# Optimization experiments

Hardware: AMD Instinct MI355X
Metric: run time of the kernel (lower is better)

The kernel has to match this reference:

```python
import jax, jax.numpy as jnp
import numpy as np


def setup_inputs() -> dict:
    key = jax.random.key(0)
    k1, k2 = jax.random.split(key)
    B, T, F, S, C = 16, 1024, 8, 128, 256
    e_src = jax.random.normal(k1, (B, T, F, C), dtype=jnp.float32)
    d_src = jax.random.randint(k2, (B, S), 0, 16, dtype=jnp.int64)
    return {"e_src": e_src, "d_src": d_src}


def reference(e_src, d_src):
    # Ragged per-phone mean pooling (the nested python loop in FastSpeech2Pros.forward):
    # e_src: [B, T_mel, F, C]; d_src: [B, S] frame durations per phone.
    # For b in range(B//2): chunk e_src[b] along T by durations, mean over (time, freq),
    # zeros for empty chunks -> agg [B//2, S, C].
    B, T, F, C = e_src.shape
    Bh = B // 2
    S = d_src.shape[1]
    e = e_src[:Bh]                      # [Bh, T, F, C]
    d = d_src[:Bh].astype(jnp.int32)    # [Bh, S]

    # frame t belongs to phone i iff cumsum(d)[i-1] <= t < cumsum(d)[i]
    cum = jnp.cumsum(d, axis=1)                                   # [Bh, S]
    t = jnp.arange(T, dtype=jnp.int32)
    seg = jax.vmap(lambda c: jnp.searchsorted(c, t, side='right'))(cum)  # [Bh, T]
    seg = jnp.minimum(seg, S)           # frames beyond total duration -> overflow bucket S

    frame_sum = e.sum(axis=2)           # [Bh, T, C] (sum over freq dim)
    sums = jax.vmap(
        lambda fs, s: jax.ops.segment_sum(fs, s, num_segments=S + 1)
    )(frame_sum, seg)[:, :S]            # [Bh, S, C]

    counts = (d * F).astype(e.dtype)    # elements per ragged chunk = dur * F
    agg = jnp.where(counts[..., None] > 0,
                    sums / jnp.maximum(counts, 1.0)[..., None],
                    jnp.zeros((), e.dtype))
    return agg
```

## Files before the change

### kernel.cpp

```cpp
#include <hip/hip_runtime.h>

#define TT 1024
#define SS 128
#define FF 8
#define CC 256
#define BH 8

__global__ __launch_bounds__(256) void fused_kernel(const float* __restrict__ e,
                                                    const int* __restrict__ dsrc,
                                                    float* __restrict__ out) {
    int s = blockIdx.x;
    int b = blockIdx.y;
    int tid = threadIdx.x;
    int c4 = tid & 63;
    int q  = tid >> 6;

    __shared__ int cumbuf[SS];
    if (tid < SS) cumbuf[tid] = dsrc[b * SS + tid];
    __syncthreads();
    #pragma unroll
    for (int off = 1; off < SS; off <<= 1) {
        int v = 0;
        if (tid < SS && tid >= off) v = cumbuf[tid - off];
        __syncthreads();
        if (tid < SS) cumbuf[tid] += v;
        __syncthreads();
    }

    int end   = cumbuf[s];
    int start = (s == 0) ? 0 : cumbuf[s - 1];
    int dc    = dsrc[b * SS + s];
    if (start > TT) start = TT;
    if (end   > TT) end   = TT;
    int K = (end - start) * FF;

    const float4* e4 = (const float4*)(e + (size_t)(b * TT + start) * (FF * CC));

    float ax = 0.f, ay = 0.f, az = 0.f, aw = 0.f;
    int k = q;
    for (; k + 12 < K; k += 16) {
        float4 v0 = e4[(size_t)(k     ) * 64 + c4];
        float4 v1 = e4[(size_t)(k +  4) * 64 + c4];
        float4 v2 = e4[(size_t)(k +  8) * 64 + c4];
        float4 v3 = e4[(size_t)(k + 12) * 64 + c4];
        ax += v0.x + v1.x + v2.x + v3.x;
        ay += v0.y + v1.y + v2.y + v3.y;
        az += v0.z + v1.z + v2.z + v3.z;
        aw += v0.w + v1.w + v2.w + v3.w;
    }
    for (; k < K; k += 4) {
        float4 v = e4[(size_t)k * 64 + c4];
        ax += v.x; ay += v.y; az += v.z; aw += v.w;
    }

    __shared__ float4 red[256];
    red[tid] = make_float4(ax, ay, az, aw);
    __syncthreads();

    if (q == 0) {
        float4 r0 = red[tid];
        float4 r1 = red[tid + 64];
        float4 r2 = red[tid + 128];
        float4 r3 = red[tid + 192];
        float inv = (dc > 0) ? (1.0f / (float)(dc * FF)) : 0.0f;
        float4 r;
        r.x = (r0.x + r1.x + r2.x + r3.x) * inv;
        r.y = (r0.y + r1.y + r2.y + r3.y) * inv;
        r.z = (r0.z + r1.z + r2.z + r3.z) * inv;
        r.w = (r0.w + r1.w + r2.w + r3.w) * inv;
        ((float4*)out)[(size_t)(b * SS + s) * 64 + c4] = r;
    }
}

extern "C" void kernel_launch(void* const* d_in, const int* in_sizes, int n_in,
                              void* d_out, int out_size, void* d_ws, size_t ws_size,
                              hipStream_t stream) {
    const float* e   = (const float*)d_in[0];
    const int*   d   = (const int*)d_in[1];
    float*       out = (float*)d_out;

    fused_kernel<<<dim3(SS, BH), 256, 0, stream>>>(e, d, out);
}
```

Measured before the change: 175.8 us.

## Split into prep and time-tiled segment-sum kernels with atomic accumulation

```diff
diff --git a/kernel.cpp b/kernel.cpp
--- a/kernel.cpp
+++ b/kernel.cpp
@@ -5,71 +5,93 @@
 #define FF 8
 #define CC 256
 #define BH 8
+#define TB 8
 
-__global__ __launch_bounds__(256) void fused_kernel(const float* __restrict__ e,
-                                                    const int* __restrict__ dsrc,
-                                                    float* __restrict__ out) {
-    int s = blockIdx.x;
-    int b = blockIdx.y;
+
+__global__ __launch_bounds__(256) void prep_kernel(const int* __restrict__ dsrc,
+                                                   int* __restrict__ segt,
+                                                   float* __restrict__ invt,
+                                                   float4* __restrict__ outz) {
     int tid = threadIdx.x;
-    int c4 = tid & 63;
-    int q  = tid >> 6;
+    int gid = blockIdx.x * 256 + tid;
+    outz[gid] = make_float4(0.f, 0.f, 0.f, 0.f);
+    if (blockIdx.x != 0) return;
 
-    __shared__ int cumbuf[SS];
-    if (tid < SS) cumbuf[tid] = dsrc[b * SS + tid];
+    __shared__ int dl[BH * SS];
+    __shared__ int cum[BH][SS];
+    for (int i = tid; i < BH * SS; i += 256) dl[i] = dsrc[i];
     __syncthreads();
-    #pragma unroll
-    for (int off = 1; off < SS; off <<= 1) {
-        int v = 0;
-        if (tid < SS && tid >= off) v = cumbuf[tid - off];
-        __syncthreads();
-        if (tid < SS) cumbuf[tid] += v;
-        __syncthreads();
+    if (tid < BH) {
+        int a = 0;
+        for (int s = 0; s < SS; ++s) { a += dl[tid * SS + s]; cum[tid][s] = a; }
+    }
+    __syncthreads();
+    for (int i = tid; i < BH * SS; i += 256) {
+        int d = dl[i];
+        invt[i] = (d > 0) ? 1.0f / (float)(d * FF) : 0.0f;
+    }
+    for (int i = tid; i < BH * TT; i += 256) {
+        int b = i >> 10, t = i & (TT - 1);
+        int lo = 0, hi = SS;
+        while (lo < hi) { int mid = (lo + hi) >> 1; if (cum[b][mid] <= t) lo = mid + 1; else hi = mid; }
+        segt[i] = lo;
+    }
+}
+
+#define FLUSH(SEG)                                                                        \
+    {                                                                                     \
+        red[tid] = acc; __syncthreads();                                                  \
+        if (tid < 64) {                                                                   \
+            float4 a0 = red[tid], a1 = red[tid + 64], a2 = red[tid + 128], a3 = red[tid + 192]; \
+            float inv = invt[b * SS + (SEG)];                                             \
+            float* o = out + ((size_t)(b * SS + (SEG)) * CC) + tid * 4;                   \
+            unsafeAtomicAdd(o + 0, (a0.x + a1.x + a2.x + a3.x) * inv);                    \
+            unsafeAtomicAdd(o + 1, (a0.y + a1.y + a2.y + a3.y) * inv);                    \
+            unsafeAtomicAdd(o + 2, (a0.z + a1.z + a2.z + a3.z) * inv);                    \
+            unsafeAtomicAdd(o + 3, (a0.w + a1.w + a2.w + a3.w) * inv);                    \
+        }                                                                                 \
+        __syncthreads();                                                                  \
     }
 
-    int end   = cumbuf[s];
-    int start = (s == 0) ? 0 : cumbuf[s - 1];
-    int dc    = dsrc[b * SS + s];
-    if (start > TT) start = TT;
-    if (end   > TT) end   = TT;
-    int K = (end - start) * FF;
+__global__ __launch_bounds__(256) void sum_kernel(const float* __restrict__ e,
+                                                  const int* __restrict__ segt,
+                                                  const float* __restrict__ invt,
+                                                  float* __restrict__ out) {
+    int t0  = blockIdx.x * TB;
+    int b   = blockIdx.y;
+    int tid = threadIdx.x;
 
-    const float4* e4 = (const float4*)(e + (size_t)(b * TT + start) * (FF * CC));
+    const int* st = segt + b * TT + t0;
+    int seg[TB];
+    #pragma unroll
+    for (int m = 0; m < TB; ++m) seg[m] = st[m];
+    if (seg[0] >= SS) return;
 
-    float ax = 0.f, ay = 0.f, az = 0.f, aw = 0.f;
-    int k = q;
-    for (; k + 12 < K; k += 16) {
-        float4 v0 = e4[(size_t)(k     ) * 64 + c4];
-        float4 v1 = e4[(size_t)(k +  4) * 64 + c4];
-        float4 v2 = e4[(size_t)(k +  8) * 64 + c4];
-        float4 v3 = e4[(size_t)(k + 12) * 64 + c4];
-        ax += v0.x + v1.x + v2.x + v3.x;
-        ay += v0.y + v1.y + v2.y + v3.y;
-        az += v0.z + v1.z + v2.z + v3.z;
-        aw += v0.w + v1.w + v2.w + v3.w;
-    }
-    for (; k < K; k += 4) {
-        float4 v = e4[(size_t)k * 64 + c4];
-        ax += v.x; ay += v.y; az += v.z; aw += v.w;
-    }
+    const float4* e4 = (const float4*)e + (size_t)(b * TT + t0) * (FF * CC / 4);
+    float4 v[16];
+    #pragma unroll
+    for (int j = 0; j < 16; ++j) v[j] = e4[j * 256 + tid];
 
     __shared__ float4 red[256];
-    red[tid] = make_float4(ax, ay, az, aw);
-    __syncthreads();
-
-    if (q == 0) {
-        float4 r0 = red[tid];
-        float4 r1 = red[tid + 64];
-        float4 r2 = red[tid + 128];
-        float4 r3 = red[tid + 192];
-        float inv = (dc > 0) ? (1.0f / (float)(dc * FF)) : 0.0f;
-        float4 r;
-        r.x = (r0.x + r1.x + r2.x + r3.x) * inv;
-        r.y = (r0.y + r1.y + r2.y + r3.y) * inv;
-        r.z = (r0.z + r1.z + r2.z + r3.z) * inv;
-        r.w = (r0.w + r1.w + r2.w + r3.w) * inv;
-        ((float4*)out)[(size_t)(b * SS + s) * 64 + c4] = r;
+    float4 acc = make_float4(0.f, 0.f, 0.f, 0.f);
+    int cur = seg[0];
+    #pragma unroll
+    for (int m = 0; m < TB; ++m) {
+        int s = seg[m];
+        if (s != cur) {
+            FLUSH(cur);
+            acc = make_float4(0.f, 0.f, 0.f, 0.f);
+            cur = s;
+        }
+        if (s < SS) {
+            float4 va = v[2 * m], vb = v[2 * m + 1];
+            acc.x += va.x + vb.x;
+            acc.y += va.y + vb.y;
+            acc.z += va.z + vb.z;
+            acc.w += va.w + vb.w;
+        }
     }
+    if (cur < SS) FLUSH(cur);
 }
 
 extern "C" void kernel_launch(void* const* d_in, const int* in_sizes, int n_in,
@@ -79,5 +101,9 @@
     const int*   d   = (const int*)d_in[1];
     float*       out = (float*)d_out;
 
-    fused_kernel<<<dim3(SS, BH), 256, 0, stream>>>(e, d, out);
+    int*   segt = (int*)d_ws;
+    float* invt = (float*)((char*)d_ws + (size_t)BH * TT * sizeof(int));
+
+    prep_kernel<<<dim3(256), 256, 0, stream>>>(d, segt, invt, (float4*)out);
+    sum_kernel<<<dim3(TT / TB, BH), 256, 0, stream>>>(e, segt, invt, out);
 }
```

Measured after the change: 193.5 us. 10.0% more time.

## Partition work by time frames with atomic accumulation into zeroed output

Applied to the files above, without the earlier changes.

```diff
diff --git a/kernel.cpp b/kernel.cpp
--- a/kernel.cpp
+++ b/kernel.cpp
@@ -5,70 +5,76 @@
 #define FF 8
 #define CC 256
 #define BH 8
+#define TB 8
+
+__global__ __launch_bounds__(256) void zero_kernel(float4* __restrict__ out) {
+    out[blockIdx.x * 256 + threadIdx.x] = make_float4(0.f, 0.f, 0.f, 0.f);
+}
+
+__device__ __forceinline__ void flush_seg(float* __restrict__ out, int b, int s,
+                                          int d0, int d1, int lane, float4 acc) {
+    int dsel = (s & 1) ? d1 : d0;
+    int ds   = __shfl(dsel, s >> 1, 64);
+    float inv = 1.0f / (float)(ds * FF);
+    float* o = out + ((size_t)(b * SS + s) * CC) + lane * 4;
+    unsafeAtomicAdd(o + 0, acc.x * inv);
+    unsafeAtomicAdd(o + 1, acc.y * inv);
+    unsafeAtomicAdd(o + 2, acc.z * inv);
+    unsafeAtomicAdd(o + 3, acc.w * inv);
+}
 
 __global__ __launch_bounds__(256) void fused_kernel(const float* __restrict__ e,
                                                     const int* __restrict__ dsrc,
                                                     float* __restrict__ out) {
-    int s = blockIdx.x;
-    int b = blockIdx.y;
-    int tid = threadIdx.x;
-    int c4 = tid & 63;
-    int q  = tid >> 6;
+    int x    = blockIdx.x;
+    int b    = blockIdx.y;
+    int tid  = threadIdx.x;
+    int lane = tid & 63;
+    int q    = tid >> 6;
 
-    __shared__ int cumbuf[SS];
-    if (tid < SS) cumbuf[tid] = dsrc[b * SS + tid];
-    __syncthreads();
+    int2 dd = ((const int2*)(dsrc + b * SS))[lane];
+    int incl = dd.x + dd.y;
     #pragma unroll
-    for (int off = 1; off < SS; off <<= 1) {
-        int v = 0;
-        if (tid < SS && tid >= off) v = cumbuf[tid - off];
-        __syncthreads();
-        if (tid < SS) cumbuf[tid] += v;
-        __syncthreads();
+    for (int off = 1; off < 64; off <<= 1) {
+        int n = __shfl_up(incl, off, 64);
+        if (lane >= off) incl += n;
+    }
+    int cumO = incl;
+    int cumE = incl - dd.y;
+
+    int tA = x * TB + 2 * q;
+    int tB = tA + 1;
+    int segA = __popcll(__ballot(cumE <= tA)) + __popcll(__ballot(cumO <= tA));
+    int segB = __popcll(__ballot(cumE <= tB)) + __popcll(__ballot(cumO <= tB));
+    bool vA = segA < SS;
+    bool vB = segB < SS;
+
+    const float4* e4 = (const float4*)e + (size_t)(b * TT + x * TB) * (FF * CC / 4);
+    const float4* w4 = e4 + (16 * q) * 64 + lane;
+
+    float4 sA = make_float4(0.f, 0.f, 0.f, 0.f);
+    float4 sB = make_float4(0.f, 0.f, 0.f, 0.f);
+    if (vA) {
+        #pragma unroll
+        for (int j = 0; j < 8; ++j) {
+            float4 v = w4[j * 64];
+            sA.x += v.x; sA.y += v.y; sA.z += v.z; sA.w += v.w;
+        }
+    }
+    if (vB) {
+        #pragma unroll
+        for (int j = 8; j < 16; ++j) {
+            float4 v = w4[j * 64];
+            sB.x += v.x; sB.y += v.y; sB.z += v.z; sB.w += v.w;
+        }
     }
 
-    int end   = cumbuf[s];
-    int start = (s == 0) ? 0 : cumbuf[s - 1];
-    int dc    = dsrc[b * SS + s];
-    if (start > TT) start = TT;
-    if (end   > TT) end   = TT;
-    int K = (end - start) * FF;
-
-    const float4* e4 = (const float4*)(e + (size_t)(b * TT + start) * (FF * CC));
-
-    float ax = 0.f, ay = 0.f, az = 0.f, aw = 0.f;
-    int k = q;
-    for (; k + 12 < K; k += 16) {
-        float4 v0 = e4[(size_t)(k     ) * 64 + c4];
-        float4 v1 = e4[(size_t)(k +  4) * 64 + c4];
-        float4 v2 = e4[(size_t)(k +  8) * 64 + c4];
-        float4 v3 = e4[(size_t)(k + 12) * 64 + c4];
-        ax += v0.x + v1.x + v2.x + v3.x;
-        ay += v0.y + v1.y + v2.y + v3.y;
-        az += v0.z + v1.z + v2.z + v3.z;
-        aw += v0.w + v1.w + v2.w + v3.w;
-    }
-    for (; k < K; k += 4) {
-        float4 v = e4[(size_t)k * 64 + c4];
-        ax += v.x; ay += v.y; az += v.z; aw += v.w;
-    }
-
-    __shared__ float4 red[256];
-    red[tid] = make_float4(ax, ay, az, aw);
-    __syncthreads();
-
-    if (q == 0) {
-        float4 r0 = red[tid];
-        float4 r1 = red[tid + 64];
-        float4 r2 = red[tid + 128];
-        float4 r3 = red[tid + 192];
-        float inv = (dc > 0) ? (1.0f / (float)(dc * FF)) : 0.0f;
-        float4 r;
-        r.x = (r0.x + r1.x + r2.x + r3.x) * inv;
-        r.y = (r0.y + r1.y + r2.y + r3.y) * inv;
-        r.z = (r0.z + r1.z + r2.z + r3.z) * inv;
-        r.w = (r0.w + r1.w + r2.w + r3.w) * inv;
-        ((float4*)out)[(size_t)(b * SS + s) * 64 + c4] = r;
+    if (vA && vB && segA == segB) {
+        sA.x += sB.x; sA.y += sB.y; sA.z += sB.z; sA.w += sB.w;
+        flush_seg(out, b, segA, dd.x, dd.y, lane, sA);
+    } else {
+        if (vA) flush_seg(out, b, segA, dd.x, dd.y, lane, sA);
+        if (vB) flush_seg(out, b, segB, dd.x, dd.y, lane, sB);
     }
 }
 
@@ -79,5 +85,6 @@
     const int*   d   = (const int*)d_in[1];
     float*       out = (float*)d_out;
 
-    fused_kernel<<<dim3(SS, BH), 256, 0, stream>>>(e, d, out);
+    zero_kernel<<<dim3(BH * SS * CC / 4 / 256), 256, 0, stream>>>((float4*)out);
+    fused_kernel<<<dim3(TT / TB, BH), 256, 0, stream>>>(e, d, out);
 }
```

Measured after the change: 182.8 us. 4.0% more time.
